# Kernel optimization log

Measured on AMD Instinct MI355X. Metric: run time of the kernel, lower is better.

The kernel has to match this reference:

```python
import jax, jax.numpy as jnp
import numpy as np

BASE_TEMP, MIN_TEMP, MAX_TEMP = 0.07, 0.04, 0.2
B, D = 4096, 768


def setup_inputs() -> dict:
    key = jax.random.key(0)
    k1, k2, k3 = jax.random.split(key, 3)
    return {
        "vision_features": jax.random.normal(k1, (B, D), dtype=jnp.float32),
        "text_features": jax.random.normal(k2, (B, D), dtype=jnp.float32),
        "match_ids": jax.random.randint(k3, (B,), 0, 1024, dtype=jnp.int64),
    }


def reference(vision_features, text_features, match_ids):
    # L2-normalize features along the feature dim
    v = vision_features / jnp.linalg.norm(vision_features, axis=1, keepdims=True)
    t = text_features / jnp.linalg.norm(text_features, axis=1, keepdims=True)
    sim = v @ t.T  # [B, B]

    n = match_ids.shape[0]
    match = match_ids[:, None] == match_ids[None, :]  # [B, B] bool, diag True
    mf = match.astype(sim.dtype)
    eye = jnp.eye(n, dtype=sim.dtype)
    pos_mask = mf * (1.0 - eye)          # diagonal zeroed
    neg_mask = 1.0 - mf                   # diagonal also zero (was match)

    pos_mean = (pos_mask * sim).sum() / jnp.maximum(1.0, pos_mask.sum())
    neg_mean = (neg_mask * sim).sum() / jnp.maximum(1.0, neg_mask.sum())
    separation = pos_mean - neg_mean
    temp = jnp.clip(BASE_TEMP * (0.8 + 0.4 * jnp.exp(-2.0 * separation)),
                    MIN_TEMP, MAX_TEMP)

    logits = sim / temp
    # v2t: for each row i, sum over positives j of (-logits[i,j] + lse(row i))
    lse_rows = jax.nn.logsumexp(logits, axis=1)  # [B]
    v2t = (mf * (lse_rows[:, None] - logits)).sum()
    # t2v: for each column i, sum over positives j of (-logits[j,i] + lse(col i))
    lse_cols = jax.nn.logsumexp(logits, axis=0)  # [B]
    t2v = (mf * (lse_cols[None, :] - logits)).sum()

    num_pos = mf.sum()  # includes diagonal, matching the torch code
    v2t = v2t / num_pos
    t2v = t2v / num_pos
    loss = (v2t + t2v) / 2.0
    return loss
```

## Files before the change

### kernel.cpp

```cpp
#include <hip/hip_runtime.h>
#include <hip/hip_bf16.h>

#define NB 4096
#define DD 768
#define NKT 12
#define NBLK 256

typedef float f32x4 __attribute__((ext_vector_type(4)));
typedef long i64x2 __attribute__((ext_vector_type(2)));
typedef unsigned int uint;

#define WAITVM(N) asm volatile("s_waitcnt vmcnt(" #N ")" ::: "memory")

__global__ void init_kernel(float* scal, uint* bars)
{
    int t = threadIdx.x;
    if (t < 16) scal[t] = 0.0f;
    bars[t] = 0u;
    bars[512 + t] = 0u;
}

__device__ __forceinline__ void grid_bar(uint* bars, uint phase, int rawb, int t)
{
    __syncthreads();
    if (t == 0) {
        int g = rawb & 15;
        uint prev = __hip_atomic_fetch_add(&bars[g * 16], 1u, __ATOMIC_ACQ_REL, __HIP_MEMORY_SCOPE_AGENT);
        if (prev == phase * 16u - 1u) {
            uint r = __hip_atomic_fetch_add(&bars[384], 1u, __ATOMIC_ACQ_REL, __HIP_MEMORY_SCOPE_AGENT);
            if (r == phase * 16u - 1u)
                __hip_atomic_store(&bars[448], phase, __ATOMIC_RELEASE, __HIP_MEMORY_SCOPE_AGENT);
        }
        while (__hip_atomic_load(&bars[448], __ATOMIC_RELAXED, __HIP_MEMORY_SCOPE_AGENT) < phase)
            __builtin_amdgcn_s_sleep(8);
        (void)__hip_atomic_load(&bars[448], __ATOMIC_ACQUIRE, __HIP_MEMORY_SCOPE_AGENT);
    }
    __syncthreads();
}

__device__ __forceinline__ void stage_range(
    unsigned char* ldsAll,
    const unsigned char* __restrict__ vhat8, const unsigned char* __restrict__ that8,
    int rowBase, int colBase, int T, int i0, int i1, int wid, int lane)
{
    int u = T & 3;
    const unsigned char* src = (wid >= 4) ? that8 : vhat8;
    int tb = (wid >= 4) ? colBase : rowBase;
    int w4 = wid & 3;
    int logc = (lane & 3) ^ ((lane >> 3) & 3);
    int rowIn = w4 * 64 + (lane >> 2);
    unsigned char* dbase = ldsAll + u * 32768 + ((wid >= 4) ? 16384 : 0) + w4 * 4096;
    #pragma unroll
    for (int i = i0; i <= i1; ++i) {
        const unsigned char* g = src + (size_t)(tb + rowIn + i * 16) * DD + T * 64 + logc * 16;
        __builtin_amdgcn_global_load_lds(
            (const __attribute__((address_space(1))) void*)g,
            (__attribute__((address_space(3))) void*)(dbase + i * 1024),
            16, 0, 0);
    }
}

__global__ __launch_bounds__(512, 2) void fused_kernel(
    const float* __restrict__ vf, const float* __restrict__ tf, const int* __restrict__ ids,
    unsigned char* __restrict__ vhat8, unsigned char* __restrict__ that8,
    float* scal, float* rs, float* cs, float* cntf, uint* bars,
    float* __restrict__ out)
{
    __shared__ unsigned char ldsAll[4 * 32768];
    __shared__ int idr[256], idc[256];
    __shared__ float red[24];
    __shared__ float rs_l[256], cs_l[256];
    __shared__ int bp[16];
    __shared__ float ra[8], rn[8];
    __shared__ float invT_sh, mf_sh;
    __shared__ uint tick_sh;

    int* np_acc = (int*)(scal + 3);
    int rawb = blockIdx.x;
    int t = threadIdx.x, wid = t >> 6, lane = t & 63;

    {
        f32x4 xr[4][3];
        uint* dsts[4];
        #pragma unroll
        for (int it = 0; it < 4; ++it) {
            int row = rawb * 32 + wid * 4 + it;
            const float* src;
            if (row < NB) { src = vf + (size_t)row * DD; dsts[it] = (uint*)(vhat8 + (size_t)row * DD); }
            else          { src = tf + (size_t)(row - NB) * DD; dsts[it] = (uint*)(that8 + (size_t)(row - NB) * DD); }
            xr[it][0] = *(const f32x4*)(src + lane * 4);
            xr[it][1] = *(const f32x4*)(src + 256 + lane * 4);
            xr[it][2] = *(const f32x4*)(src + 512 + lane * 4);
        }
        int idreg[8];
        #pragma unroll
        for (int i = 0; i < 8; ++i) idreg[i] = ids[t + i * 512];

        #pragma unroll
        for (int it = 0; it < 4; ++it) {
            float s = 0.f;
            #pragma unroll
            for (int c = 0; c < 3; ++c)
                s += xr[it][c][0]*xr[it][c][0] + xr[it][c][1]*xr[it][c][1]
                   + xr[it][c][2]*xr[it][c][2] + xr[it][c][3]*xr[it][c][3];
            #pragma unroll
            for (int off = 1; off < 64; off <<= 1) s += __shfl_xor(s, off, 64);
            float scale = 1.0f / sqrtf(s);
            #pragma unroll
            for (int c = 0; c < 3; ++c) {
                int p = __builtin_amdgcn_cvt_pk_fp8_f32(xr[it][c][0] * scale, xr[it][c][1] * scale, 0, false);
                p = __builtin_amdgcn_cvt_pk_fp8_f32(xr[it][c][2] * scale, xr[it][c][3] * scale, p, true);
                dsts[it][c * 64 + lane] = (uint)p;
            }
        }
        int* idsh = (int*)(ldsAll + 3 * 32768);
        #pragma unroll
        for (int i = 0; i < 8; ++i) idsh[t + i * 512] = idreg[i];
    }
    __syncthreads();
    if (t == 0)
        __hip_atomic_fetch_add(&bars[512 + (rawb >> 3) * 16], 1u, __ATOMIC_ACQ_REL, __HIP_MEMORY_SCOPE_AGENT);

    int rg = rawb & 7, sq = rawb >> 3;
    int by = (rg >> 1) * 4 + (sq >> 3);
    int bx = (rg & 1) * 8 + (sq & 7);
    int rowBase = by * 256, colBase = bx * 256;
    int wr = wid >> 2, wc = wid & 3;
    int fr = lane & 15, g = lane >> 4;

    if (t == 0) {
        uint* fA = &bars[512 + by * 16];
        uint* fB = &bars[512 + (16 + bx) * 16];
        while (__hip_atomic_load(fA, __ATOMIC_RELAXED, __HIP_MEMORY_SCOPE_AGENT) < 8u)
            __builtin_amdgcn_s_sleep(4);
        while (__hip_atomic_load(fB, __ATOMIC_RELAXED, __HIP_MEMORY_SCOPE_AGENT) < 8u)
            __builtin_amdgcn_s_sleep(4);
        (void)__hip_atomic_load(fA, __ATOMIC_ACQUIRE, __HIP_MEMORY_SCOPE_AGENT);
        (void)__hip_atomic_load(fB, __ATOMIC_ACQUIRE, __HIP_MEMORY_SCOPE_AGENT);
    }
    __syncthreads();

    stage_range(ldsAll, vhat8, that8, rowBase, colBase, 0, 0, 3, wid, lane);
    stage_range(ldsAll, vhat8, that8, rowBase, colBase, 1, 0, 3, wid, lane);
    stage_range(ldsAll, vhat8, that8, rowBase, colBase, 2, 0, 3, wid, lane);

    {
        int* idsh = (int*)(ldsAll + 3 * 32768);
        int sub = t >> 5, l32 = t & 31;
        int my = idsh[rawb * 16 + sub];
        const int4* idsh4 = (const int4*)idsh;
        int c = 0;
        #pragma unroll 8
        for (int j = l32; j < NB / 4; j += 32) {
            int4 v = idsh4[j];
            c += (v.x == my) + (v.y == my) + (v.z == my) + (v.w == my);
        }
        #pragma unroll
        for (int off = 16; off > 0; off >>= 1) c += __shfl_down(c, off, 32);
        if (l32 == 0) { cntf[rawb * 16 + sub] = (float)c; bp[sub] = c; }
    }
    if (t < 32) rs[rawb * 32 + t] = 0.0f;
    __syncthreads();
    if (t == 0) {
        int s = 0;
        #pragma unroll
        for (int i = 0; i < 16; ++i) s += bp[i];
        atomicAdd(np_acc, s);
    }
    WAITVM(8);
    __builtin_amdgcn_s_barrier();

    f32x4 acc[8][4];
    #pragma unroll
    for (int m = 0; m < 8; ++m)
        #pragma unroll
        for (int n = 0; n < 4; ++n) acc[m][n] = (f32x4){0.f, 0.f, 0.f, 0.f};

    int pcoff = (g ^ ((fr >> 1) & 3)) * 16;
    int aoffB = (wr * 128 + fr) * 64 + pcoff;
    int boffB = 16384 + (wc * 64 + fr) * 64 + pcoff;

    for (int T = 0; T < NKT; ++T) {
        const unsigned char* U = ldsAll + (T & 3) * 32768;
        i64x2 a0[4], bb[4];
        #pragma unroll
        for (int m = 0; m < 4; ++m) a0[m] = *(const i64x2*)(U + aoffB + m * 1024);
        #pragma unroll
        for (int n = 0; n < 4; ++n) bb[n] = *(const i64x2*)(U + boffB + n * 1024);
        if (T + 3 < NKT)
            stage_range(ldsAll, vhat8, that8, rowBase, colBase, T + 3, 0, 1, wid, lane);
        __builtin_amdgcn_s_barrier();
        __builtin_amdgcn_s_setprio(1);
        #pragma unroll
        for (int m = 0; m < 4; ++m)
            #pragma unroll
            for (int n = 0; n < 4; ++n) {
                acc[m][n] = __builtin_amdgcn_mfma_f32_16x16x32_fp8_fp8(a0[m][0], bb[n][0], acc[m][n], 0, 0, 0);
                acc[m][n] = __builtin_amdgcn_mfma_f32_16x16x32_fp8_fp8(a0[m][1], bb[n][1], acc[m][n], 0, 0, 0);
            }
        __builtin_amdgcn_s_setprio(0);
        __builtin_amdgcn_s_barrier();
        i64x2 a1[4];
        #pragma unroll
        for (int m = 0; m < 4; ++m) a1[m] = *(const i64x2*)(U + aoffB + (m + 4) * 1024);
        if (T + 3 < NKT)
            stage_range(ldsAll, vhat8, that8, rowBase, colBase, T + 3, 2, 3, wid, lane);
        __builtin_amdgcn_s_barrier();
        __builtin_amdgcn_s_setprio(1);
        #pragma unroll
        for (int m = 0; m < 4; ++m)
            #pragma unroll
            for (int n = 0; n < 4; ++n) {
                acc[m + 4][n] = __builtin_amdgcn_mfma_f32_16x16x32_fp8_fp8(a1[m][0], bb[n][0], acc[m + 4][n], 0, 0, 0);
                acc[m + 4][n] = __builtin_amdgcn_mfma_f32_16x16x32_fp8_fp8(a1[m][1], bb[n][1], acc[m + 4][n], 0, 0, 0);
            }
        __builtin_amdgcn_s_setprio(0);
        if (T < NKT - 3)       { WAITVM(8); }
        else if (T == NKT - 3) { WAITVM(4); }
        else if (T == NKT - 2) { WAITVM(0); }
        __builtin_amdgcn_s_barrier();
    }

    if (t < 256) idr[t] = ids[rowBase + t];
    else         idc[t - 256] = ids[colBase + (t - 256)];
    __syncthreads();
    {
        float tsum = 0.f, msum = 0.f, dsum = 0.f;
        #pragma unroll
        for (int m = 0; m < 8; ++m) {
            int rl = wr * 128 + m * 16 + g * 4;
            #pragma unroll
            for (int n = 0; n < 4; ++n) {
                int cl = wc * 64 + n * 16 + fr;
                int colId = idc[cl];
                int gj = colBase + cl;
                #pragma unroll
                for (int r = 0; r < 4; ++r) {
                    float val = acc[m][n][r];
                    tsum += val;
                    if (idr[rl + r] == colId) msum += val;
                    if (rowBase + rl + r == gj) dsum += val;
                }
            }
        }
        #pragma unroll
        for (int off = 32; off > 0; off >>= 1) {
            tsum += __shfl_down(tsum, off, 64);
            msum += __shfl_down(msum, off, 64);
            dsum += __shfl_down(dsum, off, 64);
        }
        if (lane == 0) { red[wid] = tsum; red[8 + wid] = msum; red[16 + wid] = dsum; }
        __syncthreads();
        if (t == 0) {
            float s0 = 0.f, s1 = 0.f, s2 = 0.f;
            #pragma unroll
            for (int w = 0; w < 8; ++w) { s0 += red[w]; s1 += red[8 + w]; s2 += red[16 + w]; }
            atomicAdd(&scal[0], s0);
            atomicAdd(&scal[1], s1);
            atomicAdd(&scal[2], s2);
        }
    }
    if (t < 256) { rs_l[t] = 0.0f; cs_l[t] = 0.0f; }

    grid_bar(bars, 1u, rawb, t);

    if (t == 0) {
        int npi = __hip_atomic_load(np_acc, __ATOMIC_RELAXED, __HIP_MEMORY_SCOPE_AGENT);
        float total = __hip_atomic_load(&scal[0], __ATOMIC_RELAXED, __HIP_MEMORY_SCOPE_AGENT);
        float mf    = __hip_atomic_load(&scal[1], __ATOMIC_RELAXED, __HIP_MEMORY_SCOPE_AGENT);
        float trace = __hip_atomic_load(&scal[2], __ATOMIC_RELAXED, __HIP_MEMORY_SCOPE_AGENT);
        float np = (float)npi;
        float pos_cnt = np - (float)NB;
        float neg_cnt = (float)NB * (float)NB - np;
        float pos_mean = (mf - trace) / fmaxf(1.0f, pos_cnt);
        float neg_mean = (total - mf) / fmaxf(1.0f, neg_cnt);
        float sep = pos_mean - neg_mean;
        float temp = 0.07f * (0.8f + 0.4f * expf(-2.0f * sep));
        temp = fminf(fmaxf(temp, 0.04f), 0.2f);
        invT_sh = 1.0f / temp;
        mf_sh = mf;
    }
    __syncthreads();
    float invT = invT_sh;

    #pragma unroll
    for (int m = 0; m < 8; ++m)
        #pragma unroll
        for (int n = 0; n < 4; ++n)
            #pragma unroll
            for (int r = 0; r < 4; ++r)
                acc[m][n][r] = __expf((acc[m][n][r] - 1.0f) * invT);
    #pragma unroll
    for (int m = 0; m < 8; ++m) {
        #pragma unroll
        for (int r = 0; r < 4; ++r) {
            float rp = 0.f;
            #pragma unroll
            for (int n = 0; n < 4; ++n) rp += acc[m][n][r];
            rp += __shfl_xor(rp, 1, 64);
            rp += __shfl_xor(rp, 2, 64);
            rp += __shfl_xor(rp, 4, 64);
            rp += __shfl_xor(rp, 8, 64);
            if (fr == 0) atomicAdd(&rs_l[wr * 128 + m * 16 + g * 4 + r], rp);
        }
    }
    #pragma unroll
    for (int n = 0; n < 4; ++n) {
        float cp = 0.f;
        #pragma unroll
        for (int m = 0; m < 8; ++m)
            #pragma unroll
            for (int r = 0; r < 4; ++r) cp += acc[m][n][r];
        cp += __shfl_xor(cp, 16, 64);
        cp += __shfl_xor(cp, 32, 64);
        if (g == 0) atomicAdd(&cs_l[wc * 64 + n * 16 + fr], cp);
    }
    __syncthreads();
    if (t < 256) {
        atomicAdd(&rs[rowBase + t], rs_l[t]);
        atomicAdd(&cs[colBase + t], cs_l[t]);
    }

    __syncthreads();
    if (t == 0) {
        uint prev = __hip_atomic_fetch_add(&bars[464], 1u, __ATOMIC_ACQ_REL, __HIP_MEMORY_SCOPE_AGENT);
        tick_sh = prev;
    }
    __syncthreads();
    if (tick_sh != NBLK - 1) return;

    {
        float a = 0.f, npl = 0.f;
        for (int i = t; i < NB; i += 512) {
            float cf = cntf[i];
            a += cf * (logf(rs[i]) + logf(cs[i]));
            npl += cf;
        }
        #pragma unroll
        for (int off = 32; off > 0; off >>= 1) {
            a += __shfl_down(a, off, 64);
            npl += __shfl_down(npl, off, 64);
        }
        if (lane == 0) { ra[wid] = a; rn[wid] = npl; }
        __syncthreads();
        if (t == 0) {
            float A = 0.f, np = 0.f;
            #pragma unroll
            for (int w = 0; w < 8; ++w) { A += ra[w]; np += rn[w]; }
            out[0] = (A + 2.0f * invT_sh * (np - mf_sh)) / (2.0f * np);
        }
    }
}

extern "C" void kernel_launch(void* const* d_in, const int* in_sizes, int n_in,
                              void* d_out, int out_size, void* d_ws, size_t ws_size,
                              hipStream_t stream)
{
    const float* vf  = (const float*)d_in[0];
    const float* tf  = (const float*)d_in[1];
    const int*   ids = (const int*)d_in[2];

    float* ws_f = (float*)d_ws;
    float* scal = ws_f;
    float* rs   = ws_f + 16;
    float* cs   = ws_f + 16 + 4096;
    float* cntf = ws_f + 16 + 8192;
    uint* bars  = (uint*)(ws_f + 16 + 12800);
    unsigned char* vhat8 = (unsigned char*)d_ws + 131072;
    unsigned char* that8 = vhat8 + (size_t)NB * DD;

    init_kernel<<<1, 512, 0, stream>>>(scal, bars);
    fused_kernel<<<NBLK, 512, 0, stream>>>(vf, tf, ids, vhat8, that8,
                                           scal, rs, cs, cntf, bars, (float*)d_out);
}
```

Baseline: 76.13 us.

## Distribute final log-sum reduction across row/column-finishing blocks instead of last block

Replaces the single last-block tail reduction over all 4096 rows and columns with per-row-strip and per-column-strip completion counters. The block that finishes a strip reduces that strip's 256 logf terms and adds the result atomically, and a final counter picks which block writes the output. Match-id staging into LDS is also moved earlier, reading from the already-loaded shared ids instead of global memory after the GEMM. The aim is to shorten the serial tail, at the cost of extra atomics and float-atomic ordering nondeterminism.

```diff
diff --git a/kernel.cpp b/kernel.cpp
--- a/kernel.cpp
+++ b/kernel.cpp
@@ -18,6 +18,8 @@
     if (t < 16) scal[t] = 0.0f;
     bars[t] = 0u;
     bars[512 + t] = 0u;
+    bars[1024 + t] = 0u;
+    bars[1536 + t] = 0u;
 }
 
 __device__ __forceinline__ void grid_bar(uint* bars, uint phase, int rawb, int t)
@@ -71,11 +73,12 @@
     __shared__ float red[24];
     __shared__ float rs_l[256], cs_l[256];
     __shared__ int bp[16];
-    __shared__ float ra[8], rn[8];
     __shared__ float invT_sh, mf_sh;
-    __shared__ uint tick_sh;
+    __shared__ int fin_sh;
+    __shared__ float fra[8];
 
     int* np_acc = (int*)(scal + 3);
+    float* A_acc = scal + 4;
     int rawb = blockIdx.x;
     int t = threadIdx.x, wid = t >> 6, lane = t & 63;
 
@@ -158,6 +161,8 @@
         #pragma unroll
         for (int off = 16; off > 0; off >>= 1) c += __shfl_down(c, off, 32);
         if (l32 == 0) { cntf[rawb * 16 + sub] = (float)c; bp[sub] = c; }
+        if (t < 256) idr[t] = idsh[rowBase + t];
+        else         idc[t - 256] = idsh[colBase + (t - 256)];
     }
     if (t < 32) rs[rawb * 32 + t] = 0.0f;
     __syncthreads();
@@ -221,9 +226,6 @@
         __builtin_amdgcn_s_barrier();
     }
 
-    if (t < 256) idr[t] = ids[rowBase + t];
-    else         idc[t - 256] = ids[colBase + (t - 256)];
-    __syncthreads();
     {
         float tsum = 0.f, msum = 0.f, dsum = 0.f;
         #pragma unroll
@@ -323,30 +325,35 @@
 
     __syncthreads();
     if (t == 0) {
-        uint prev = __hip_atomic_fetch_add(&bars[464], 1u, __ATOMIC_ACQ_REL, __HIP_MEMORY_SCOPE_AGENT);
-        tick_sh = prev;
-    }
-    __syncthreads();
-    if (tick_sh != NBLK - 1) return;
-
-    {
-        float a = 0.f, npl = 0.f;
-        for (int i = t; i < NB; i += 512) {
-            float cf = cntf[i];
-            a += cf * (logf(rs[i]) + logf(cs[i]));
-            npl += cf;
-        }
-        #pragma unroll
-        for (int off = 32; off > 0; off >>= 1) {
-            a += __shfl_down(a, off, 64);
-            npl += __shfl_down(npl, off, 64);
-        }
-        if (lane == 0) { ra[wid] = a; rn[wid] = npl; }
-        __syncthreads();
-        if (t == 0) {
-            float A = 0.f, np = 0.f;
-            #pragma unroll
-            for (int w = 0; w < 8; ++w) { A += ra[w]; np += rn[w]; }
+        int k = 0;
+        uint pr = __hip_atomic_fetch_add(&bars[1024 + by * 16], 1u, __ATOMIC_ACQ_REL, __HIP_MEMORY_SCOPE_AGENT);
+        if (pr == 15u) k |= 1;
+        uint pc = __hip_atomic_fetch_add(&bars[1536 + bx * 16], 1u, __ATOMIC_ACQ_REL, __HIP_MEMORY_SCOPE_AGENT);
+        if (pc == 15u) k |= 2;
+        fin_sh = k;
+    }
+    __syncthreads();
+    int kfin = fin_sh;
+    if (kfin == 0) return;
+
+    float partial = 0.f;
+    if ((kfin & 1) && t < 256) partial += cntf[rowBase + t] * logf(rs[rowBase + t]);
+    if ((kfin & 2) && t < 256) partial += cntf[colBase + t] * logf(cs[colBase + t]);
+    #pragma unroll
+    for (int off = 32; off > 0; off >>= 1) partial += __shfl_down(partial, off, 64);
+    if (lane == 0) fra[wid] = partial;
+    __syncthreads();
+    if (t == 0) {
+        float bsum = 0.f;
+        #pragma unroll
+        for (int w = 0; w < 8; ++w) bsum += fra[w];
+        atomicAdd(A_acc, bsum);
+        uint inc = (kfin == 3) ? 2u : 1u;
+        uint prevd = __hip_atomic_fetch_add(&bars[464], inc, __ATOMIC_ACQ_REL, __HIP_MEMORY_SCOPE_AGENT);
+        if (prevd + inc == 32u) {
+            float A  = __hip_atomic_load(A_acc, __ATOMIC_RELAXED, __HIP_MEMORY_SCOPE_AGENT);
+            int npi  = __hip_atomic_load(np_acc, __ATOMIC_RELAXED, __HIP_MEMORY_SCOPE_AGENT);
+            float np = (float)npi;
             out[0] = (A + 2.0f * invT_sh * (np - mf_sh)) / (2.0f * np);
         }
     }
```

After: 77.88 us. 1.02x slower.
